# Kernel tuning notes

Measured on AMD Instinct MI355X. Metric: run time of the kernel, lower is better.

Reference implementation:

```python
import jax, jax.numpy as jnp
import numpy as np

NEG_INF = -1000000.0  # matches torch masked_fill constant


def setup_inputs() -> dict:
    key = jax.random.key(0)
    k1, k2, k3, k4 = jax.random.split(key, 4)
    B, Lq, Lk, d = 64, 1024, 1024, 64
    queries = jax.random.normal(k1, (B, Lq, d), dtype=jnp.float32)
    keys = jax.random.normal(k2, (B, Lk, d), dtype=jnp.float32)
    values = jax.random.normal(k3, (B, Lk, d), dtype=jnp.float32)
    valid_lens = jax.random.randint(k4, (B,), 0, 1024, dtype=jnp.int64)
    return {"queries": queries, "keys": keys, "values": values, "valid_lens": valid_lens}


def reference(queries, keys, values, valid_lens):
    d = queries.shape[-1]
    # [B, Lq, Lk] scores
    scores = jnp.einsum("bqd,bkd->bqk", queries, keys) / jnp.sqrt(jnp.float32(d))
    Lk = scores.shape[-1]
    # valid_lens is per-batch (dim 1 in torch): same mask across all query rows
    mask = jnp.arange(Lk)[None, None, :] < valid_lens[:, None, None]  # [B,1,Lk]
    scores = jnp.where(mask, scores, NEG_INF)
    attn = jax.nn.softmax(scores, axis=-1)
    # dropout p=0.0 -> identity
    return jnp.einsum("bqk,bkd->bqd", attn, values)
```

## Files before the change

kernel.cpp:

```cpp
#include <hip/hip_runtime.h>
#include <hip/hip_bf16.h>

#define NEG_BIG -1000000.0f

typedef __attribute__((ext_vector_type(8))) short short8;
typedef __attribute__((ext_vector_type(4))) short short4v;
typedef __attribute__((ext_vector_type(4))) float floatx4;

#if __has_builtin(__builtin_amdgcn_exp2f)
#define EXP2F(x) __builtin_amdgcn_exp2f(x)
#else
#define EXP2F(x) exp2f(x)
#endif

#if __has_builtin(__builtin_amdgcn_mfma_f32_16x16x16bf16_1k)
#define MFMA16(a, b, c) __builtin_amdgcn_mfma_f32_16x16x16bf16_1k(a, b, c, 0, 0, 0)
#else
static __device__ __forceinline__ floatx4 MFMA16_fn(short4v a, short4v b, floatx4 c) {
    floatx4 d;
    asm("v_mfma_f32_16x16x16_bf16 %0, %1, %2, %3\n\ts_nop 4"
        : "=v"(d) : "v"(a), "v"(b), "v"(c));
    return d;
}
#define MFMA16(a, b, c) MFMA16_fn(a, b, c)
#endif

#if __has_builtin(__builtin_amdgcn_permlane16_swap) && __has_builtin(__builtin_amdgcn_permlane32_swap)
static __device__ __forceinline__ float redmax16_32(float x) {
    auto a = __builtin_amdgcn_permlane16_swap(__float_as_int(x), __float_as_int(x), false, false);
    x = fmaxf(__int_as_float(a[0]), __int_as_float(a[1]));
    auto b = __builtin_amdgcn_permlane32_swap(__float_as_int(x), __float_as_int(x), false, false);
    return fmaxf(__int_as_float(b[0]), __int_as_float(b[1]));
}
static __device__ __forceinline__ float redsum16_32(float x) {
    auto a = __builtin_amdgcn_permlane16_swap(__float_as_int(x), __float_as_int(x), false, false);
    x = __int_as_float(a[0]) + __int_as_float(a[1]);
    auto b = __builtin_amdgcn_permlane32_swap(__float_as_int(x), __float_as_int(x), false, false);
    return __int_as_float(b[0]) + __int_as_float(b[1]);
}
#else
static __device__ __forceinline__ float redmax16_32(float x) {
    x = fmaxf(x, __shfl_xor(x, 16));
    return fmaxf(x, __shfl_xor(x, 32));
}
static __device__ __forceinline__ float redsum16_32(float x) {
    x += __shfl_xor(x, 16);
    return x + __shfl_xor(x, 32);
}
#endif

static __device__ __forceinline__ unsigned short bf16u(float f) {
    union { __hip_bfloat16 h; unsigned short u; } c;
    c.h = __float2bfloat16(f);
    return c.u;
}

static __device__ __forceinline__ short8 pack8(float4 a, float4 b) {
    union { short8 s; __hip_bfloat162 h[4]; } u;
    u.h[0] = __float22bfloat162_rn(make_float2(a.x, a.y));
    u.h[1] = __float22bfloat162_rn(make_float2(a.z, a.w));
    u.h[2] = __float22bfloat162_rn(make_float2(b.x, b.y));
    u.h[3] = __float22bfloat162_rn(make_float2(b.z, b.w));
    return u.s;
}

__global__ __launch_bounds__(512, 4)
void attn_fwd(const float* __restrict__ Q, const float* __restrict__ K,
              const float* __restrict__ V, const int* __restrict__ vlen,
              float* __restrict__ out)
{
    __shared__ __attribute__((aligned(16))) unsigned short K_lds[2][4096];
    __shared__ __attribute__((aligned(16))) unsigned short VT_lds[3][4096];

    const int bid  = blockIdx.x;
    const int orig = (bid & 7) * 64 + (bid >> 3);
    const int b    = orig >> 3;
    const int qc   = orig & 7;

    const int tid = threadIdx.x;
    const int l   = tid & 63;
    const int w   = tid >> 6;
    const int lr  = l & 15;
    const int lg  = l >> 4;

    const float* Qb = Q + (size_t)b * 65536;
    const float* Kb = K + (size_t)b * 65536;
    const float* Vb = V + (size_t)b * 65536;

    const int valid = vlen[b];
    const int kmax  = (valid == 0) ? 1024 : valid;
    const int ntile = (kmax + 63) >> 6;

    const float qscale = 0.18033688011112042f;
    short8 qf[2];
#pragma unroll
    for (int c = 0; c < 2; ++c) {
        const float* p = Qb + (size_t)(qc*128 + w*16 + lr) * 64 + c*32 + lg*8;
        float4 a = *(const float4*)p, bb = *(const float4*)(p + 4);
        a.x *= qscale; a.y *= qscale; a.z *= qscale; a.w *= qscale;
        bb.x *= qscale; bb.y *= qscale; bb.z *= qscale; bb.w *= qscale;
        qf[c] = pack8(a, bb);
    }

    floatx4 o[4];
#pragma unroll
    for (int n = 0; n < 4; ++n) o[n] = (floatx4){0.f, 0.f, 0.f, 0.f};
    float m = -INFINITY, lsum = 0.f;
    short4v pkp[4];

    const int row   = tid >> 3;
    const int cbase = (tid & 7) * 8;

    float4 kra[2], vra[2];

#define LOAD_K(T) do {                                                      \
    const float* pk_ = Kb + (size_t)((T)*64 + row) * 64 + cbase;            \
    kra[0] = *(const float4*)pk_;  kra[1] = *(const float4*)(pk_ + 4);      \
    } while (0)

#define LOAD_V(T) do {                                                      \
    const float* pv_ = Vb + (size_t)((T)*64 + row) * 64 + cbase;            \
    vra[0] = *(const float4*)pv_;  vra[1] = *(const float4*)(pv_ + 4);      \
    } while (0)

#define WRITE_K(B) do {                                                     \
    const int _fk = (row & 7) * 8;                                          \
    *(short8*)&K_lds[B][row*64 + (cbase ^ _fk)] = pack8(kra[0], kra[1]);    \
    } while (0)

#define WRITE_V(B) do {                                                     \
    _Pragma("unroll")                                                       \
    for (int j = 0; j < 8; ++j) {                                           \
        const int dv = cbase + j;                                           \
        const int fv = ((dv & 7) ^ (dv >> 3)) * 8;                          \
        VT_lds[B][dv*64 + (row ^ fv)] = bf16u(((const float*)&vra[j>>2])[j&3]); \
    } } while (0)

#define QK_MFMA(SA, KBUF) do {                                              \
    _Pragma("unroll")                                                       \
    for (int n = 0; n < 4; ++n) {                                           \
        const int kr_ = n*16 + lr;                                          \
        const int fk_ = (lr & 7) * 8;                                       \
        const short8 kf0 = *(const short8*)&K_lds[KBUF][kr_*64 + ((lg*8)      ^ fk_)]; \
        const short8 kf1 = *(const short8*)&K_lds[KBUF][kr_*64 + ((32 + lg*8) ^ fk_)]; \
        SA[n] = (floatx4){0.f, 0.f, 0.f, 0.f};                              \
        SA[n] = __builtin_amdgcn_mfma_f32_16x16x32_bf16(kf0, qf[0], SA[n], 0, 0, 0); \
        SA[n] = __builtin_amdgcn_mfma_f32_16x16x32_bf16(kf1, qf[1], SA[n], 0, 0, 0); \
    } } while (0)

#define PV_MFMA(VBUF) do {                                                  \
    _Pragma("unroll")                                                       \
    for (int kc = 0; kc < 4; ++kc) {                                        \
        _Pragma("unroll")                                                   \
        for (int n2 = 0; n2 < 4; ++n2) {                                    \
            const int dv_ = n2*16 + lr;                                     \
            const int fv_ = ((dv_ & 7) ^ (dv_ >> 3)) * 8;                   \
            const short4v vf = *(const short4v*)&VT_lds[VBUF][dv_*64 + ((kc*16 + lg*4) ^ fv_)]; \
            o[n2] = MFMA16(pkp[kc], vf, o[n2]);                             \
        }                                                                   \
    } } while (0)

#define SOFTMAX(SA, T) do {                                                 \
    const int _k0 = (T) * 64;                                               \
    if ((_k0 + 64) > valid) {                                               \
        const int kb_ = _k0 + lg*4;                                         \
        _Pragma("unroll")                                                   \
        for (int n = 0; n < 4; ++n)                                         \
        _Pragma("unroll")                                                   \
        for (int r = 0; r < 4; ++r)                                         \
            SA[n][r] = (kb_ + n*16 + r >= valid) ? NEG_BIG : SA[n][r];      \
    }                                                                       \
                                      \
    float m0_ = fmaxf(fmaxf(SA[0][0], SA[0][1]), SA[0][2]);                 \
    float m1_ = fmaxf(fmaxf(SA[0][3], SA[1][0]), SA[1][1]);                 \
    float m2_ = fmaxf(fmaxf(SA[1][2], SA[1][3]), SA[2][0]);                 \
    float m3_ = fmaxf(fmaxf(SA[2][1], SA[2][2]), SA[2][3]);                 \
    float m4_ = fmaxf(fmaxf(SA[3][0], SA[3][1]), SA[3][2]);                 \
    float rmax = fmaxf(fmaxf(fmaxf(m0_, m1_), fmaxf(m2_, m3_)),            \
                       fmaxf(m4_, SA[3][3]));                               \
    rmax = redmax16_32(rmax);                                               \
    if (!__all(rmax <= m + 11.0f)) {                                        \
        const float nm_ = fmaxf(m, rmax);                                   \
        const float sc_f = EXP2F(m - nm_);                                  \
        m = nm_;                                                            \
        lsum *= sc_f;                                                       \
        float sc_r[4];                                                      \
        _Pragma("unroll")                                                   \
        for (int r = 0; r < 4; ++r) sc_r[r] = __shfl(sc_f, lg*4 + r);       \
        _Pragma("unroll")                                                   \
        for (int n = 0; n < 4; ++n)                                         \
        _Pragma("unroll")                                                   \
        for (int r = 0; r < 4; ++r) o[n][r] *= sc_r[r];                     \
    }                                                                       \
    _Pragma("unroll")                                                       \
    for (int n = 0; n < 4; ++n)                                             \
    _Pragma("unroll")                                                       \
    for (int r = 0; r < 4; ++r) SA[n][r] = EXP2F(SA[n][r] - m);             \
                                            \
    float s0_ = (SA[0][0]+SA[0][1]) + (SA[0][2]+SA[0][3]);                  \
    float s1_ = (SA[1][0]+SA[1][1]) + (SA[1][2]+SA[1][3]);                  \
    float s2_ = (SA[2][0]+SA[2][1]) + (SA[2][2]+SA[2][3]);                  \
    float s3_ = (SA[3][0]+SA[3][1]) + (SA[3][2]+SA[3][3]);                  \
    lsum += redsum16_32((s0_ + s1_) + (s2_ + s3_));                         \
    _Pragma("unroll")                                                       \
    for (int n = 0; n < 4; ++n) {                                           \
        union { short4v s; __hip_bfloat162 h[2]; } u;                       \
        u.h[0] = __float22bfloat162_rn(make_float2(SA[n][0], SA[n][1]));    \
        u.h[1] = __float22bfloat162_rn(make_float2(SA[n][2], SA[n][3]));    \
        pkp[n] = u.s;                                                       \
    } } while (0)

    LOAD_K(0);
    LOAD_V(0);
    WRITE_K(0);
    WRITE_V(0);
    __syncthreads();

    {
        if (ntile > 1) { LOAD_K(1); LOAD_V(1); }
        floatx4 sc[4];
        __builtin_amdgcn_s_setprio(1);
        QK_MFMA(sc, 0);
        __builtin_amdgcn_s_setprio(0);
        if (ntile > 1) { WRITE_K(1); WRITE_V(1); }
        SOFTMAX(sc, 0);
        if (ntile > 1) __syncthreads();
    }

    int vr = 0, vw = 2;
    for (int t = 1; t < ntile; ++t) {
        const bool pf = (t + 1 < ntile);
        if (pf) { LOAD_K(t + 1); LOAD_V(t + 1); }

        floatx4 sc[4];
        __builtin_amdgcn_s_setprio(1);
        QK_MFMA(sc, t & 1);
        PV_MFMA(vr);
        __builtin_amdgcn_s_setprio(0);

        if (pf) { WRITE_K((t + 1) & 1); WRITE_V(vw); }
        SOFTMAX(sc, t);
        __syncthreads();

        vr = (vr == 2) ? 0 : vr + 1;
        vw = (vw == 2) ? 0 : vw + 1;
    }

    __builtin_amdgcn_s_setprio(1);
    PV_MFMA(vr);
    __builtin_amdgcn_s_setprio(0);

    const float inv = 1.0f / lsum;
    float inv_r[4];
#pragma unroll
    for (int r = 0; r < 4; ++r) inv_r[r] = __shfl(inv, lg*4 + r);

    float* Ob = out + (size_t)b * 65536;
#pragma unroll
    for (int n = 0; n < 4; ++n)
#pragma unroll
    for (int r = 0; r < 4; ++r) {
        const int q = qc*128 + w*16 + lg*4 + r;
        Ob[(size_t)q * 64 + n*16 + lr] = o[n][r] * inv_r[r];
    }
#undef LOAD_K
#undef LOAD_V
#undef WRITE_K
#undef WRITE_V
#undef QK_MFMA
#undef PV_MFMA
#undef SOFTMAX
}

extern "C" void kernel_launch(void* const* d_in, const int* in_sizes, int n_in,
                              void* d_out, int out_size, void* d_ws, size_t ws_size,
                              hipStream_t stream) {
    (void)in_sizes; (void)n_in; (void)d_ws; (void)ws_size; (void)out_size;
    const float* Q  = (const float*)d_in[0];
    const float* K  = (const float*)d_in[1];
    const float* V  = (const float*)d_in[2];
    const int*   vl = (const int*)d_in[3];
    float* O = (float*)d_out;
    attn_fwd<<<dim3(512), dim3(512), 0, stream>>>(Q, K, V, vl, O);
}
```

Measured before the change: 37.47 us.

## Process K/V tiles in pairs to halve barriers and restructure softmax-PV pipeline

```diff
diff --git a/kernel.cpp b/kernel.cpp
--- a/kernel.cpp
+++ b/kernel.cpp
@@ -69,8 +69,8 @@
               const float* __restrict__ V, const int* __restrict__ vlen,
               float* __restrict__ out)
 {
-    __shared__ __attribute__((aligned(16))) unsigned short K_lds[2][4096];
-    __shared__ __attribute__((aligned(16))) unsigned short VT_lds[3][4096];
+    __shared__ __attribute__((aligned(16))) unsigned short K_lds[2][2][4096];
+    __shared__ __attribute__((aligned(16))) unsigned short VT_lds[2][2][4096];
 
     const int bid  = blockIdx.x;
     const int orig = (bid & 7) * 64 + (bid >> 3);
@@ -90,6 +90,7 @@
     const int valid = vlen[b];
     const int kmax  = (valid == 0) ? 1024 : valid;
     const int ntile = (kmax + 63) >> 6;
+    const int npair = (ntile + 1) >> 1;
 
     const float qscale = 0.18033688011112042f;
     short8 qf[2];
@@ -106,61 +107,51 @@
 #pragma unroll
     for (int n = 0; n < 4; ++n) o[n] = (floatx4){0.f, 0.f, 0.f, 0.f};
     float m = -INFINITY, lsum = 0.f;
-    short4v pkp[4];
 
     const int row   = tid >> 3;
     const int cbase = (tid & 7) * 8;
 
-    float4 kra[2], vra[2];
-
-#define LOAD_K(T) do {                                                      \
-    const float* pk_ = Kb + (size_t)((T)*64 + row) * 64 + cbase;            \
-    kra[0] = *(const float4*)pk_;  kra[1] = *(const float4*)(pk_ + 4);      \
+    float4 krA[2], krB[2], vrA[2], vrB[2];
+
+#define LOAD_PAIR(P) do {                                                   \
+    const float* pkA = Kb + (size_t)((P)*128 + row) * 64 + cbase;           \
+    krA[0] = *(const float4*)pkA;  krA[1] = *(const float4*)(pkA + 4);      \
+    const float* pkB = pkA + 64*64;                                         \
+    krB[0] = *(const float4*)pkB;  krB[1] = *(const float4*)(pkB + 4);      \
+    const float* pvA = Vb + (size_t)((P)*128 + row) * 64 + cbase;           \
+    vrA[0] = *(const float4*)pvA;  vrA[1] = *(const float4*)(pvA + 4);      \
+    const float* pvB = pvA + 64*64;                                         \
+    vrB[0] = *(const float4*)pvB;  vrB[1] = *(const float4*)(pvB + 4);      \
     } while (0)
 
-#define LOAD_V(T) do {                                                      \
-    const float* pv_ = Vb + (size_t)((T)*64 + row) * 64 + cbase;            \
-    vra[0] = *(const float4*)pv_;  vra[1] = *(const float4*)(pv_ + 4);      \
-    } while (0)
-
-#define WRITE_K(B) do {                                                     \
+#define WRITE_PAIR(B) do {                                                  \
     const int _fk = (row & 7) * 8;                                          \
-    *(short8*)&K_lds[B][row*64 + (cbase ^ _fk)] = pack8(kra[0], kra[1]);    \
-    } while (0)
-
-#define WRITE_V(B) do {                                                     \
+    *(short8*)&K_lds[B][0][row*64 + (cbase ^ _fk)] = pack8(krA[0], krA[1]); \
+    *(short8*)&K_lds[B][1][row*64 + (cbase ^ _fk)] = pack8(krB[0], krB[1]); \
     _Pragma("unroll")                                                       \
     for (int j = 0; j < 8; ++j) {                                           \
         const int dv = cbase + j;                                           \
         const int fv = ((dv & 7) ^ (dv >> 3)) * 8;                          \
-        VT_lds[B][dv*64 + (row ^ fv)] = bf16u(((const float*)&vra[j>>2])[j&3]); \
+        VT_lds[B][0][dv*64 + (row ^ fv)] = bf16u(((const float*)&vrA[j>>2])[j&3]); \
+        VT_lds[B][1][dv*64 + (row ^ fv)] = bf16u(((const float*)&vrB[j>>2])[j&3]); \
     } } while (0)
 
-#define QK_MFMA(SA, KBUF) do {                                              \
+#define QK_MFMA(SA, BUF, S) do {                                            \
+    __builtin_amdgcn_s_setprio(1);                                          \
     _Pragma("unroll")                                                       \
     for (int n = 0; n < 4; ++n) {                                           \
         const int kr_ = n*16 + lr;                                          \
         const int fk_ = (lr & 7) * 8;                                       \
-        const short8 kf0 = *(const short8*)&K_lds[KBUF][kr_*64 + ((lg*8)      ^ fk_)]; \
-        const short8 kf1 = *(const short8*)&K_lds[KBUF][kr_*64 + ((32 + lg*8) ^ fk_)]; \
+        const short8 kf0 = *(const short8*)&K_lds[BUF][S][kr_*64 + ((lg*8)      ^ fk_)]; \
+        const short8 kf1 = *(const short8*)&K_lds[BUF][S][kr_*64 + ((32 + lg*8) ^ fk_)]; \
         SA[n] = (floatx4){0.f, 0.f, 0.f, 0.f};                              \
         SA[n] = __builtin_amdgcn_mfma_f32_16x16x32_bf16(kf0, qf[0], SA[n], 0, 0, 0); \
         SA[n] = __builtin_amdgcn_mfma_f32_16x16x32_bf16(kf1, qf[1], SA[n], 0, 0, 0); \
-    } } while (0)
-
-#define PV_MFMA(VBUF) do {                                                  \
-    _Pragma("unroll")                                                       \
-    for (int kc = 0; kc < 4; ++kc) {                                        \
-        _Pragma("unroll")                                                   \
-        for (int n2 = 0; n2 < 4; ++n2) {                                    \
-            const int dv_ = n2*16 + lr;                                     \
-            const int fv_ = ((dv_ & 7) ^ (dv_ >> 3)) * 8;                   \
-            const short4v vf = *(const short4v*)&VT_lds[VBUF][dv_*64 + ((kc*16 + lg*4) ^ fv_)]; \
-            o[n2] = MFMA16(pkp[kc], vf, o[n2]);                             \
-        }                                                                   \
-    } } while (0)
-
-#define SOFTMAX(SA, T) do {                                                 \
+    }                                                                       \
+    __builtin_amdgcn_s_setprio(0);                                          \
+    } while (0)
+
+#define SM_PV(SA, T, BUF, S) do {                                           \
     const int _k0 = (T) * 64;                                               \
     if ((_k0 + 64) > valid) {                                               \
         const int kb_ = _k0 + lg*4;                                         \
@@ -196,59 +187,54 @@
     for (int n = 0; n < 4; ++n)                                             \
     _Pragma("unroll")                                                       \
     for (int r = 0; r < 4; ++r) SA[n][r] = EXP2F(SA[n][r] - m);             \
-                                            \
     float s0_ = (SA[0][0]+SA[0][1]) + (SA[0][2]+SA[0][3]);                  \
     float s1_ = (SA[1][0]+SA[1][1]) + (SA[1][2]+SA[1][3]);                  \
     float s2_ = (SA[2][0]+SA[2][1]) + (SA[2][2]+SA[2][3]);                  \
     float s3_ = (SA[3][0]+SA[3][1]) + (SA[3][2]+SA[3][3]);                  \
     lsum += redsum16_32((s0_ + s1_) + (s2_ + s3_));                         \
+    short4v pk_[4];                                                         \
     _Pragma("unroll")                                                       \
     for (int n = 0; n < 4; ++n) {                                           \
-        union { short4v s; __hip_bfloat162 h[2]; } u;                       \
+        union { short4v v; __hip_bfloat162 h[2]; } u;                       \
         u.h[0] = __float22bfloat162_rn(make_float2(SA[n][0], SA[n][1]));    \
         u.h[1] = __float22bfloat162_rn(make_float2(SA[n][2], SA[n][3]));    \
-        pkp[n] = u.s;                                                       \
-    } } while (0)
-
-    LOAD_K(0);
-    LOAD_V(0);
-    WRITE_K(0);
-    WRITE_V(0);
+        pk_[n] = u.v;                                                       \
+    }                                                                       \
+    __builtin_amdgcn_s_setprio(1);                                          \
+    _Pragma("unroll")                                                       \
+    for (int kc = 0; kc < 4; ++kc) {                                        \
+        _Pragma("unroll")                                                   \
+        for (int n2 = 0; n2 < 4; ++n2) {                                    \
+            const int dv_ = n2*16 + lr;                                     \
+            const int fv_ = ((dv_ & 7) ^ (dv_ >> 3)) * 8;                   \
+            const short4v vf = *(const short4v*)&VT_lds[BUF][S][dv_*64 + ((kc*16 + lg*4) ^ fv_)]; \
+            o[n2] = MFMA16(pk_[kc], vf, o[n2]);                             \
+        }                                                                   \
+    }                                                                       \
+    __builtin_amdgcn_s_setprio(0);                                          \
+    } while (0)
+
+    LOAD_PAIR(0);
+    WRITE_PAIR(0);
     __syncthreads();
 
-    {
-        if (ntile > 1) { LOAD_K(1); LOAD_V(1); }
-        floatx4 sc[4];
-        __builtin_amdgcn_s_setprio(1);
-        QK_MFMA(sc, 0);
-        __builtin_amdgcn_s_setprio(0);
-        if (ntile > 1) { WRITE_K(1); WRITE_V(1); }
-        SOFTMAX(sc, 0);
-        if (ntile > 1) __syncthreads();
+    for (int p = 0; p < npair; ++p) {
+        const int buf = p & 1;
+        const bool pf = (p + 1 < npair);
+        if (pf) LOAD_PAIR(p + 1);
+
+        floatx4 sa[4];
+        QK_MFMA(sa, buf, 0);
+        SM_PV(sa, 2*p, buf, 0);
+
+        if (2*p + 1 < ntile) {
+            QK_MFMA(sa, buf, 1);
+            SM_PV(sa, 2*p + 1, buf, 1);
+        }
+
+        if (pf) WRITE_PAIR(buf ^ 1);
+        __syncthreads();
     }
-
-    int vr = 0, vw = 2;
-    for (int t = 1; t < ntile; ++t) {
-        const bool pf = (t + 1 < ntile);
-        if (pf) { LOAD_K(t + 1); LOAD_V(t + 1); }
-
-        floatx4 sc[4];
-        __builtin_amdgcn_s_setprio(1);
-        QK_MFMA(sc, t & 1);
-        PV_MFMA(vr);
-        __builtin_amdgcn_s_setprio(0);
-
-        if (pf) { WRITE_K((t + 1) & 1); WRITE_V(vw); }
-        SOFTMAX(sc, t);
-        __syncthreads();
-
-        vr = (vr == 2) ? 0 : vr + 1;
-        vw = (vw == 2) ? 0 : vw + 1;
-    }
-
-    __builtin_amdgcn_s_setprio(1);
-    PV_MFMA(vr);
-    __builtin_amdgcn_s_setprio(0);
 
     const float inv = 1.0f / lsum;
     float inv_r[4];
@@ -263,13 +249,10 @@
         const int q = qc*128 + w*16 + lg*4 + r;
         Ob[(size_t)q * 64 + n*16 + lr] = o[n][r] * inv_r[r];
     }
-#undef LOAD_K
-#undef LOAD_V
-#undef WRITE_K
-#undef WRITE_V
+#undef LOAD_PAIR
+#undef WRITE_PAIR
 #undef QK_MFMA
-#undef PV_MFMA
-#undef SOFTMAX
+#undef SM_PV
 }
 
 extern "C" void kernel_launch(void* const* d_in, const int* in_sizes, int n_in,
```

Result: slower. 44.75 us (+19.4%).
